# Kernel optimization log

Hardware: AMD Instinct MI355X
Metric: run time of the kernel (lower is better)

## Reference

```python
import jax, jax.numpy as jnp
import numpy as np

B = 65536
D_IN = 8
H1, H2 = 256, 256


def setup_inputs() -> dict:
    key = jax.random.key(0)
    ks = jax.random.split(key, 12)
    def lin(kw, kb, fan_in, fan_out):
        s = 1.0 / np.sqrt(fan_in)
        W = jax.random.uniform(kw, (fan_out, fan_in), jnp.float32, -s, s)
        b = jax.random.uniform(kb, (fan_out,), jnp.float32, -s, s)
        return W, b
    W0, b0 = lin(ks[0], ks[1], D_IN, H1)
    W1, b1 = lin(ks[2], ks[3], H1, H2)
    W2, b2 = lin(ks[4], ks[5], H2, 1)
    W3, b3 = lin(ks[6], ks[7], 1, 8)
    x_batch = jax.random.normal(ks[8], (B, D_IN), jnp.float32)
    scores_x_batch = jax.random.normal(ks[9], (B, D_IN), jnp.float32)
    c = jnp.zeros((), jnp.float32)  # init_val parameter
    return {"x_batch": x_batch, "scores_x_batch": scores_x_batch,
            "W0": W0, "b0": b0, "W1": W1, "b1": b1,
            "W2": W2, "b2": b2, "W3": W3, "b3": b3, "c": c}


def reference(x_batch, scores_x_batch, W0, b0, W1, b1, W2, b2, W3, b3, c):
    # singleforwardpass: tanh on all layers except the last
    def single(x):  # x: [8] -> [8]
        y = jnp.tanh(W0 @ x + b0)
        y = jnp.tanh(W1 @ y + b1)
        y = jnp.tanh(W2 @ y + b2)
        return W3 @ y + b3

    eye = jnp.eye(D_IN, dtype=x_batch.dtype)

    def per_sample(x, score):
        # jacobian(single, x).diag().sum() + dot(single(x), score) + c
        u, lin_fn = jax.linearize(single, x)
        J = jax.vmap(lin_fn)(eye)        # [8, 8] (columns of Jacobian as rows)
        div = jnp.trace(J)               # sum of Jacobian diagonal
        return c + div + jnp.dot(u, score)

    return jax.vmap(per_sample)(x_batch, scores_x_batch)  # [B]
```

## Files before the change

### kernel.cpp

```cpp
#include <hip/hip_runtime.h>
#include <hip/hip_bf16.h>

#define B_TOTAL 65536
#define H 256
#define TS 64
#define THREADS 512
#define STRIDE 264

typedef __attribute__((ext_vector_type(8))) short bf16x8;
typedef __attribute__((ext_vector_type(4))) float f32x4;

__device__ __forceinline__ void tanh_r(float x, float& t, float& r) {
    float e = __expf(x + x);
    r = __builtin_amdgcn_rcpf(e + 1.0f);
    t = fmaf(-2.0f, r, 1.0f);
}
__device__ __forceinline__ float bf2f(ushort b) {
    union { unsigned u; float f; } v; v.u = ((unsigned)b) << 16;
    return v.f;
}
__device__ __forceinline__ ushort f2bf(float f) {
    union { float f; unsigned u; } v; v.f = f;
    unsigned r = v.u + 0x7fffu + ((v.u >> 16) & 1u);
    return (ushort)(r >> 16);
}
__device__ __forceinline__ ushort2 cvt2(float a, float b) {
    union { __hip_bfloat162 h; ushort2 u; } v;
    v.h = __float22bfloat162_rn(make_float2(a, b));
    return v.u;
}
__device__ __forceinline__ bf16x8 pack8(float4 a, float4 b) {
    union { bf16x8 v; ushort2 u[4]; } r;
    r.u[0] = cvt2(a.x, a.y); r.u[1] = cvt2(a.z, a.w);
    r.u[2] = cvt2(b.x, b.y); r.u[3] = cvt2(b.z, b.w);
    return r.v;
}

__global__ void pack_weights(const float* __restrict__ W1, ushort* __restrict__ pack) {
    int g = blockIdx.x * 256 + threadIdx.x;
    int jt = g >> 9;
    int ks = (g >> 6) & 7;
    int l  = g & 63;
    int row = jt * 16 + (l & 15);
    int k0  = ks * 32 + (l >> 4) * 8;
    ushort* dst = pack + (size_t)g * 8;
    const float* src = W1 + (size_t)row * H + k0;
#pragma unroll
    for (int t = 0; t < 8; ++t) dst[t] = f2bf(src[t]);
}

__launch_bounds__(THREADS, 4)
__global__ void fused_mlp(const float* __restrict__ x_batch,
                          const float* __restrict__ scores,
                          const float* __restrict__ W0, const float* __restrict__ b0,
                          const float* __restrict__ b1,
                          const float* __restrict__ W2, const float* __restrict__ b2,
                          const float* __restrict__ W3, const float* __restrict__ b3,
                          const float* __restrict__ cptr,
                          const ushort* __restrict__ packs,
                          float* __restrict__ out) {
    __shared__ ushort Y0[TS][STRIDE];
    __shared__ ushort DG[TS][STRIDE];
    __shared__ float  G0[H];
    __shared__ float  Z2p[8][TS];
    __shared__ float  Trp[8][TS];

    const int tid  = threadIdx.x;
    const int lane = tid & 63;
    const int w    = tid >> 6;
    const int bs   = blockIdx.x * TS;
    const int cl   = lane & 15;
    const int q    = lane >> 4;
    const int rq   = q * 4;
    const int j0   = w * 32;

    const ushort* pW = packs + (size_t)(2 * w) * 4096 + (size_t)lane * 8;

    if (tid < H) {
        const float* wr = W0 + (size_t)tid * 8;
        float4 wa = *(const float4*)wr, wb = *(const float4*)(wr + 4);
        float4 w3a = *(const float4*)W3, w3b = *(const float4*)(W3 + 4);
        G0[tid] = wa.x * w3a.x + wa.y * w3a.y + wa.z * w3a.z + wa.w * w3a.w
                + wb.x * w3b.x + wb.y * w3b.y + wb.z * w3b.z + wb.w * w3b.w;
    }

    f32x4 l0[2][4];
    {
        bf16x8 bx[4];
#pragma unroll
        for (int st = 0; st < 4; ++st) {
            bf16x8 p = (bf16x8){0, 0, 0, 0, 0, 0, 0, 0};
            if (q == 0) {
                const float* xr = x_batch + (size_t)(bs + st * 16 + cl) * 8;
                p = pack8(*(const float4*)xr, *(const float4*)(xr + 4));
            }
            bx[st] = p;
        }
        const float* wr0 = W0 + (size_t)(j0 + cl) * 8;
        const float* wr1 = W0 + (size_t)(j0 + 16 + cl) * 8;
        bf16x8 af0 = pack8(*(const float4*)wr0, *(const float4*)(wr0 + 4));
        bf16x8 af1 = pack8(*(const float4*)wr1, *(const float4*)(wr1 + 4));
#pragma unroll
        for (int st = 0; st < 4; ++st) {
            f32x4 z = (f32x4){0.f, 0.f, 0.f, 0.f};
            l0[0][st] = __builtin_amdgcn_mfma_f32_16x16x32_bf16(af0, bx[st], z, 0, 0, 0);
            l0[1][st] = __builtin_amdgcn_mfma_f32_16x16x32_bf16(af1, bx[st], z, 0, 0, 0);
        }
    }
    __syncthreads();

    {
        float4 b0v0 = *(const float4*)(b0 + j0 + rq);
        float4 b0v1 = *(const float4*)(b0 + j0 + 16 + rq);
        float4 g0v0 = *(const float4*)&G0[j0 + rq];
        float4 g0v1 = *(const float4*)&G0[j0 + 16 + rq];
#pragma unroll
        for (int st = 0; st < 4; ++st) {
            const int row = st * 16 + cl;
#pragma unroll
            for (int jt = 0; jt < 2; ++jt) {
                f32x4 z = l0[jt][st];
                float4 bv = jt ? b0v1 : b0v0;
                float4 gv = jt ? g0v1 : g0v0;
                float t0, t1, t2, t3, r0, r1, r2, r3;
                tanh_r(z[0] + bv.x, t0, r0); tanh_r(z[1] + bv.y, t1, r1);
                tanh_r(z[2] + bv.z, t2, r2); tanh_r(z[3] + bv.w, t3, r3);
                ushort2 lo = cvt2(t0, t1), hi = cvt2(t2, t3);
                ushort4 vv; vv.x = lo.x; vv.y = lo.y; vv.z = hi.x; vv.w = hi.y;
                *(ushort4*)&Y0[row][j0 + jt * 16 + rq] = vv;
                float m0 = 4.f * r0, m1 = 4.f * r1, m2 = 4.f * r2, m3 = 4.f * r3;
                float d0 = fmaf(-m0, r0, m0), d1 = fmaf(-m1, r1, m1);
                float d2 = fmaf(-m2, r2, m2), d3 = fmaf(-m3, r3, m3);
                lo = cvt2(d0 * gv.x, d1 * gv.y); hi = cvt2(d2 * gv.z, d3 * gv.w);
                vv.x = lo.x; vv.y = lo.y; vv.z = hi.x; vv.w = hi.y;
                *(ushort4*)&DG[row][j0 + jt * 16 + rq] = vv;
            }
        }
    }
    __syncthreads();

    f32x4 facc[2][4], bacc[2][4];
#pragma unroll
    for (int jt = 0; jt < 2; ++jt)
#pragma unroll
        for (int st = 0; st < 4; ++st) {
            facc[jt][st] = (f32x4){0.f, 0.f, 0.f, 0.f};
            bacc[jt][st] = (f32x4){0.f, 0.f, 0.f, 0.f};
        }
#pragma unroll
    for (int ks = 0; ks < 8; ++ks) {
        const int k0 = ks * 32 + q * 8;
        bf16x8 wf0 = *(const bf16x8*)(pW + (size_t)ks * 512);
        bf16x8 wf1 = *(const bf16x8*)(pW + 4096 + (size_t)ks * 512);
#pragma unroll
        for (int st = 0; st < 4; ++st) {
            bf16x8 by = *(const bf16x8*)&Y0[st * 16 + cl][k0];
            bf16x8 bd = *(const bf16x8*)&DG[st * 16 + cl][k0];
            facc[0][st] = __builtin_amdgcn_mfma_f32_16x16x32_bf16(wf0, by, facc[0][st], 0, 0, 0);
            facc[1][st] = __builtin_amdgcn_mfma_f32_16x16x32_bf16(wf1, by, facc[1][st], 0, 0, 0);
            bacc[0][st] = __builtin_amdgcn_mfma_f32_16x16x32_bf16(wf0, bd, bacc[0][st], 0, 0, 0);
            bacc[1][st] = __builtin_amdgcn_mfma_f32_16x16x32_bf16(wf1, bd, bacc[1][st], 0, 0, 0);
        }
    }

    {
        float4 b1v0 = *(const float4*)(b1 + j0 + rq);
        float4 b1v1 = *(const float4*)(b1 + j0 + 16 + rq);
        float4 w2v0 = *(const float4*)(W2 + j0 + rq);
        float4 w2v1 = *(const float4*)(W2 + j0 + 16 + rq);
#pragma unroll
        for (int st = 0; st < 4; ++st) {
            float zp = 0.f, tp = 0.f;
#pragma unroll
            for (int jt = 0; jt < 2; ++jt) {
                f32x4 z  = facc[jt][st];
                f32x4 mm = bacc[jt][st];
                float4 bv = jt ? b1v1 : b1v0;
                float4 wv = jt ? w2v1 : w2v0;
                float t0, t1, t2, t3, r0, r1, r2, r3;
                tanh_r(z[0] + bv.x, t0, r0); tanh_r(z[1] + bv.y, t1, r1);
                tanh_r(z[2] + bv.z, t2, r2); tanh_r(z[3] + bv.w, t3, r3);
                zp = fmaf(wv.x, t0, zp); zp = fmaf(wv.y, t1, zp);
                zp = fmaf(wv.z, t2, zp); zp = fmaf(wv.w, t3, zp);
                float m0 = 4.f * wv.x * r0, m1 = 4.f * wv.y * r1;
                float m2 = 4.f * wv.z * r2, m3 = 4.f * wv.w * r3;
                float a0 = fmaf(-m0, r0, m0), a1 = fmaf(-m1, r1, m1);
                float a2 = fmaf(-m2, r2, m2), a3 = fmaf(-m3, r3, m3);
                tp = fmaf(a0, mm[0], tp); tp = fmaf(a1, mm[1], tp);
                tp = fmaf(a2, mm[2], tp); tp = fmaf(a3, mm[3], tp);
            }
            zp += __shfl_xor(zp, 16);
            zp += __shfl_xor(zp, 32);
            tp += __shfl_xor(tp, 16);
            tp += __shfl_xor(tp, 32);
            if (lane < 16) {
                Z2p[w][st * 16 + lane] = zp;
                Trp[w][st * 16 + lane] = tp;
            }
        }
    }
    __syncthreads();

    if (tid < TS) {
        const int s = tid;
        float z2 = b2[0], tr = 0.f;
#pragma unroll
        for (int k = 0; k < 8; ++k) { z2 += Z2p[k][s]; tr += Trp[k][s]; }
        float y2, r2;
        tanh_r(z2, y2, r2);
        float m2 = 4.0f * r2;
        float dy2 = fmaf(-m2, r2, m2);
        float4 w3a = *(const float4*)W3;
        float4 w3b = *(const float4*)(W3 + 4);
        float4 b3a = *(const float4*)b3;
        float4 b3b = *(const float4*)(b3 + 4);
        const float* sc = scores + (size_t)(bs + s) * 8;
        float4 s0 = *(const float4*)sc;
        float4 s1 = *(const float4*)(sc + 4);
        float p1 = w3a.x * s0.x + w3a.y * s0.y + w3a.z * s0.z + w3a.w * s0.w
                 + w3b.x * s1.x + w3b.y * s1.y + w3b.z * s1.z + w3b.w * s1.w;
        float p2 = b3a.x * s0.x + b3a.y * s0.y + b3a.z * s0.z + b3a.w * s0.w
                 + b3b.x * s1.x + b3b.y * s1.y + b3b.z * s1.z + b3b.w * s1.w;
        out[bs + s] = cptr[0] + dy2 * tr + fmaf(y2, p1, p2);
    }
}

extern "C" void kernel_launch(void* const* d_in, const int* in_sizes, int n_in,
                              void* d_out, int out_size, void* d_ws, size_t ws_size,
                              hipStream_t stream) {
    const float* x  = (const float*)d_in[0];
    const float* sc = (const float*)d_in[1];
    const float* W0 = (const float*)d_in[2];
    const float* b0 = (const float*)d_in[3];
    const float* W1 = (const float*)d_in[4];
    const float* b1 = (const float*)d_in[5];
    const float* W2 = (const float*)d_in[6];
    const float* b2 = (const float*)d_in[7];
    const float* W3 = (const float*)d_in[8];
    const float* b3 = (const float*)d_in[9];
    const float* c  = (const float*)d_in[10];
    float* out = (float*)d_out;
    ushort* packs = (ushort*)d_ws;

    hipLaunchKernelGGL(pack_weights, dim3(32), dim3(256), 0, stream, W1, packs);
    hipLaunchKernelGGL(fused_mlp, dim3(B_TOTAL / TS), dim3(THREADS), 0, stream,
                       x, sc, W0, b0, b1, W2, b2, W3, b3, c, packs, out);
}
```

Baseline: 34.15 us.

## Retile layer-2 MFMA warps to 64 outputs by 32 samples with weight prefetch

Changes the warp-to-tile mapping of the second-layer GEMM. Each warp now covers 64 output neurons for half of the 64 samples, instead of 32 neurons for all samples. This halves the LDS reads of the Y0/DG activation fragments per warp, since each fragment now feeds 8 MFMAs instead of 4. It also software-prefetches the next k-step's weight fragments from global memory with a rolled loop. In exchange each warp holds more weight registers and the k-loop is no longer unrolled, which may raise register pressure and add loop overhead.

```diff
diff --git a/kernel.cpp b/kernel.cpp
--- a/kernel.cpp
+++ b/kernel.cpp
@@ -62,8 +62,8 @@
     __shared__ ushort Y0[TS][STRIDE];
     __shared__ ushort DG[TS][STRIDE];
     __shared__ float  G0[H];
-    __shared__ float  Z2p[8][TS];
-    __shared__ float  Trp[8][TS];
+    __shared__ float  Z2p[4][TS];
+    __shared__ float  Trp[4][TS];
 
     const int tid  = threadIdx.x;
     const int lane = tid & 63;
@@ -73,8 +73,10 @@
     const int q    = lane >> 4;
     const int rq   = q * 4;
     const int j0   = w * 32;
-
-    const ushort* pW = packs + (size_t)(2 * w) * 4096 + (size_t)lane * 8;
+    const int wj   = w & 3;
+    const int sb   = (w >> 2) * 32;
+
+    const ushort* pW = packs + (size_t)(4 * wj) * 4096 + (size_t)lane * 8;
 
     if (tid < H) {
         const float* wr = W0 + (size_t)tid * 8;
@@ -137,46 +139,65 @@
             }
         }
     }
+
+    bf16x8 wf0_ = *(const bf16x8*)(pW);
+    bf16x8 wf1_ = *(const bf16x8*)(pW + 4096);
+    bf16x8 wf2_ = *(const bf16x8*)(pW + 8192);
+    bf16x8 wf3_ = *(const bf16x8*)(pW + 12288);
+
     __syncthreads();
 
-    f32x4 facc[2][4], bacc[2][4];
-#pragma unroll
-    for (int jt = 0; jt < 2; ++jt)
-#pragma unroll
-        for (int st = 0; st < 4; ++st) {
-            facc[jt][st] = (f32x4){0.f, 0.f, 0.f, 0.f};
-            bacc[jt][st] = (f32x4){0.f, 0.f, 0.f, 0.f};
-        }
-#pragma unroll
+    f32x4 facc[4][2], bacc[4][2];
+#pragma unroll
+    for (int jj = 0; jj < 4; ++jj)
+#pragma unroll
+        for (int stl = 0; stl < 2; ++stl) {
+            facc[jj][stl] = (f32x4){0.f, 0.f, 0.f, 0.f};
+            bacc[jj][stl] = (f32x4){0.f, 0.f, 0.f, 0.f};
+        }
+#pragma unroll 1
     for (int ks = 0; ks < 8; ++ks) {
+        bf16x8 wn0 = wf0_, wn1 = wf1_, wn2 = wf2_, wn3 = wf3_;
+        if (ks < 7) {
+            const ushort* pn = pW + (size_t)(ks + 1) * 512;
+            wn0 = *(const bf16x8*)(pn);
+            wn1 = *(const bf16x8*)(pn + 4096);
+            wn2 = *(const bf16x8*)(pn + 8192);
+            wn3 = *(const bf16x8*)(pn + 12288);
+        }
         const int k0 = ks * 32 + q * 8;
-        bf16x8 wf0 = *(const bf16x8*)(pW + (size_t)ks * 512);
-        bf16x8 wf1 = *(const bf16x8*)(pW + 4096 + (size_t)ks * 512);
-#pragma unroll
-        for (int st = 0; st < 4; ++st) {
-            bf16x8 by = *(const bf16x8*)&Y0[st * 16 + cl][k0];
-            bf16x8 bd = *(const bf16x8*)&DG[st * 16 + cl][k0];
-            facc[0][st] = __builtin_amdgcn_mfma_f32_16x16x32_bf16(wf0, by, facc[0][st], 0, 0, 0);
-            facc[1][st] = __builtin_amdgcn_mfma_f32_16x16x32_bf16(wf1, by, facc[1][st], 0, 0, 0);
-            bacc[0][st] = __builtin_amdgcn_mfma_f32_16x16x32_bf16(wf0, bd, bacc[0][st], 0, 0, 0);
-            bacc[1][st] = __builtin_amdgcn_mfma_f32_16x16x32_bf16(wf1, bd, bacc[1][st], 0, 0, 0);
-        }
+#pragma unroll
+        for (int stl = 0; stl < 2; ++stl) {
+            bf16x8 by = *(const bf16x8*)&Y0[sb + stl * 16 + cl][k0];
+            bf16x8 bd = *(const bf16x8*)&DG[sb + stl * 16 + cl][k0];
+            facc[0][stl] = __builtin_amdgcn_mfma_f32_16x16x32_bf16(wf0_, by, facc[0][stl], 0, 0, 0);
+            bacc[0][stl] = __builtin_amdgcn_mfma_f32_16x16x32_bf16(wf0_, bd, bacc[0][stl], 0, 0, 0);
+            facc[1][stl] = __builtin_amdgcn_mfma_f32_16x16x32_bf16(wf1_, by, facc[1][stl], 0, 0, 0);
+            bacc[1][stl] = __builtin_amdgcn_mfma_f32_16x16x32_bf16(wf1_, bd, bacc[1][stl], 0, 0, 0);
+            facc[2][stl] = __builtin_amdgcn_mfma_f32_16x16x32_bf16(wf2_, by, facc[2][stl], 0, 0, 0);
+            bacc[2][stl] = __builtin_amdgcn_mfma_f32_16x16x32_bf16(wf2_, bd, bacc[2][stl], 0, 0, 0);
+            facc[3][stl] = __builtin_amdgcn_mfma_f32_16x16x32_bf16(wf3_, by, facc[3][stl], 0, 0, 0);
+            bacc[3][stl] = __builtin_amdgcn_mfma_f32_16x16x32_bf16(wf3_, bd, bacc[3][stl], 0, 0, 0);
+        }
+        wf0_ = wn0; wf1_ = wn1; wf2_ = wn2; wf3_ = wn3;
     }
 
     {
-        float4 b1v0 = *(const float4*)(b1 + j0 + rq);
-        float4 b1v1 = *(const float4*)(b1 + j0 + 16 + rq);
-        float4 w2v0 = *(const float4*)(W2 + j0 + rq);
-        float4 w2v1 = *(const float4*)(W2 + j0 + 16 + rq);
-#pragma unroll
-        for (int st = 0; st < 4; ++st) {
+        float4 b1v[4], w2v[4];
+#pragma unroll
+        for (int jj = 0; jj < 4; ++jj) {
+            b1v[jj] = *(const float4*)(b1 + wj * 64 + jj * 16 + rq);
+            w2v[jj] = *(const float4*)(W2 + wj * 64 + jj * 16 + rq);
+        }
+#pragma unroll
+        for (int stl = 0; stl < 2; ++stl) {
             float zp = 0.f, tp = 0.f;
 #pragma unroll
-            for (int jt = 0; jt < 2; ++jt) {
-                f32x4 z  = facc[jt][st];
-                f32x4 mm = bacc[jt][st];
-                float4 bv = jt ? b1v1 : b1v0;
-                float4 wv = jt ? w2v1 : w2v0;
+            for (int jj = 0; jj < 4; ++jj) {
+                f32x4 z  = facc[jj][stl];
+                f32x4 mm = bacc[jj][stl];
+                float4 bv = b1v[jj];
+                float4 wv = w2v[jj];
                 float t0, t1, t2, t3, r0, r1, r2, r3;
                 tanh_r(z[0] + bv.x, t0, r0); tanh_r(z[1] + bv.y, t1, r1);
                 tanh_r(z[2] + bv.z, t2, r2); tanh_r(z[3] + bv.w, t3, r3);
@@ -194,8 +215,8 @@
             tp += __shfl_xor(tp, 16);
             tp += __shfl_xor(tp, 32);
             if (lane < 16) {
-                Z2p[w][st * 16 + lane] = zp;
-                Trp[w][st * 16 + lane] = tp;
+                Z2p[wj][sb + stl * 16 + lane] = zp;
+                Trp[wj][sb + stl * 16 + lane] = tp;
             }
         }
     }
@@ -205,7 +226,7 @@
         const int s = tid;
         float z2 = b2[0], tr = 0.f;
 #pragma unroll
-        for (int k = 0; k < 8; ++k) { z2 += Z2p[k][s]; tr += Trp[k][s]; }
+        for (int k = 0; k < 4; ++k) { z2 += Z2p[k][s]; tr += Trp[k][s]; }
         float y2, r2;
         tanh_r(z2, y2, r2);
         float m2 = 4.0f * r2;
```

New measurement: 35.05 us. 1.03x slower.
